# Performance work log

Hardware: AMD Instinct MI355X
Metric: run time of the kernel (lower is better)

## Reference

```python
import jax, jax.numpy as jnp
import numpy as np

EMBED_DIM = 1024
HEAD_DIM = 64


def setup_inputs() -> dict:
    key = jax.random.key(0)
    ks = jax.random.split(key, 7)
    B, S = 4, 2048
    x = jax.random.normal(ks[0], (B, S, EMBED_DIM), dtype=jnp.float32)
    s = EMBED_DIM ** -0.5  # torch Linear default init scale (uniform bound)
    Wk = jax.random.uniform(ks[1], (EMBED_DIM, HEAD_DIM), minval=-s, maxval=s)
    bk = jax.random.uniform(ks[2], (HEAD_DIM,), minval=-s, maxval=s)
    Wq = jax.random.uniform(ks[3], (EMBED_DIM, HEAD_DIM), minval=-s, maxval=s)
    bq = jax.random.uniform(ks[4], (HEAD_DIM,), minval=-s, maxval=s)
    Wv = jax.random.uniform(ks[5], (EMBED_DIM, HEAD_DIM), minval=-s, maxval=s)
    bv = jax.random.uniform(ks[6], (HEAD_DIM,), minval=-s, maxval=s)
    return {"x": x, "Wq": Wq, "bq": bq, "Wk": Wk, "bk": bk, "Wv": Wv, "bv": bv}


def reference(x, Wq, bq, Wk, bk, Wv, bv):
    # projections: [B,S,D]
    q = x @ Wq + bq
    k = x @ Wk + bk
    v = x @ Wv + bv
    # NOTE: faithful to source, which DIVIDES by head_dim**-0.5 (i.e. multiplies by sqrt(d))
    scale = HEAD_DIM ** -0.5
    wei = jnp.einsum('bqd,bkd->bqk', q, k) / scale  # [B,S,S]
    S = x.shape[1]
    causal = jnp.tril(jnp.ones((S, S), dtype=bool))
    wei = jnp.where(causal, wei, -jnp.inf)
    attn_weights = jax.nn.softmax(wei, axis=-1)
    return jnp.einsum('bqk,bkd->bqd', attn_weights, v)
```

## Files before the change

### kernel.cpp

```cpp
#include <hip/hip_runtime.h>
#include <math.h>

#define S_LEN 2048
#define NB 4
#define EMB 1024
#define HD 64
#define NROW (NB * S_LEN)
#define NEG_BIG -3.0e38f
#define SC 11.5415603f
#define DEFER_THR 3.0f
#define KVSPLIT 4

typedef _Float16 half8 __attribute__((ext_vector_type(8)));
typedef _Float16 half4 __attribute__((ext_vector_type(4)));
typedef float f32x4 __attribute__((ext_vector_type(4)));

static __device__ __forceinline__ f32x4 mfma32(half8 a, half8 b, f32x4 c) {
    return __builtin_amdgcn_mfma_f32_16x16x32_f16(a, b, c, 0, 0, 0);
}
static __device__ __forceinline__ f32x4 mfma16(half4 a, half4 b, f32x4 c) {
    return __builtin_amdgcn_mfma_f32_16x16x16f16(a, b, c, 0, 0, 0);
}

__global__ __launch_bounds__(256) void prep_w(
    const float* __restrict__ Wq, const float* __restrict__ Wk,
    const float* __restrict__ Wv, _Float16* __restrict__ wt_frag)
{
    const int g  = blockIdx.x >> 4;
    const int kc = blockIdx.x & 15;
    const int k0 = kc * 64;
    const float* W = (g == 0) ? Wq : (g == 1) ? Wk : Wv;

    __shared__ float tile[64][68];
    const int t = threadIdx.x;
    {
        const int kk = t >> 2, cb = (t & 3) * 16;
#pragma unroll
        for (int i = 0; i < 4; i++)
            *(f32x4*)&tile[kk][cb + 4 * i] =
                *(const f32x4*)(W + (size_t)(k0 + kk) * HD + cb + 4 * i);
    }
    __syncthreads();

    const int c4 = t >> 6, l = t & 63;
    const int col = c4 * 16 + (l & 15);
    const int krow = (l >> 4) * 8;
#pragma unroll
    for (int sub = 0; sub < 2; sub++) {
        half8 hv;
#pragma unroll
        for (int e = 0; e < 8; e++)
            hv[e] = (_Float16)tile[sub * 32 + krow + e][col];
        const size_t addr = (size_t)(g * 4 + c4) * 16384 +
                            (size_t)(kc * 2 + sub) * 512 + (size_t)l * 8;
        *(half8*)(wt_frag + addr) = hv;
    }
}

__global__ __launch_bounds__(768) void proj_kernel(
    const float* __restrict__ x, const _Float16* __restrict__ wt_frag,
    const float* __restrict__ bq, const float* __restrict__ bk,
    const float* __restrict__ bv,
    _Float16* __restrict__ qs, _Float16* __restrict__ kh_,
    _Float16* __restrict__ vt)
{
    const int m0 = blockIdx.x * 32;
    const int t = threadIdx.x, lane = t & 63, w = t >> 6;

    __shared__ __align__(16) _Float16 xs[32][1032];

    for (int i = t; i < 4096; i += 768) {
        const int row = i >> 7, off = (i & 127) * 8;
        const float* xp = x + (size_t)(m0 + row) * EMB + off;
        const f32x4 v0 = *(const f32x4*)xp;
        const f32x4 v1 = *(const f32x4*)(xp + 4);
        half8 h;
#pragma unroll
        for (int jj = 0; jj < 4; jj++) {
            h[jj]     = (_Float16)v0[jj];
            h[4 + jj] = (_Float16)v1[jj];
        }
        *(half8*)&xs[row][off] = h;
    }

    const int f = w;
    const int row0 = lane & 15, kq = lane >> 4;
    const _Float16* wp = wt_frag + (size_t)f * 16384 + (size_t)lane * 8;

    half8 wbuf[4];
#pragma unroll
    for (int c = 0; c < 4; c++) wbuf[c] = *(const half8*)(wp + (size_t)c * 512);

    __syncthreads();

    f32x4 acc0 = f32x4{0, 0, 0, 0}, acc1 = f32x4{0, 0, 0, 0};

#pragma unroll
    for (int c = 0; c < 32; ++c) {
        const half8 ax0 = *(const half8*)&xs[row0][c * 32 + kq * 8];
        const half8 ax1 = *(const half8*)&xs[16 + row0][c * 32 + kq * 8];
        const half8 bw = wbuf[c & 3];
        acc0 = mfma32(ax0, bw, acc0);
        acc1 = mfma32(ax1, bw, acc1);
        if (c + 4 < 32) wbuf[c & 3] = *(const half8*)(wp + (size_t)(c + 4) * 512);
    }

    const int mat = f >> 2, c4 = f & 3;
    const int mcol = c4 * 16 + (lane & 15);
    const float bb = ((mat == 0) ? bq : (mat == 1) ? bk : bv)[mcol];
#pragma unroll
    for (int rh = 0; rh < 2; rh++) {
        const f32x4 acc = rh ? acc1 : acc0;
        const int grow0 = m0 + rh * 16 + kq * 4;
        if (mat == 0) {
#pragma unroll
            for (int r = 0; r < 4; r++)
                qs[(size_t)(grow0 + r) * HD + mcol] = (_Float16)((acc[r] + bb) * SC);
        } else if (mat == 1) {
#pragma unroll
            for (int r = 0; r < 4; r++)
                kh_[(size_t)(grow0 + r) * HD + mcol] = (_Float16)(acc[r] + bb);
        } else {
            half4 hv;
#pragma unroll
            for (int r = 0; r < 4; r++) hv[r] = (_Float16)(acc[r] + bb);
            const int bidx = grow0 >> 11, sr = grow0 & (S_LEN - 1);
            *(half4*)(vt + ((size_t)bidx * HD + mcol) * S_LEN + sr) = hv;
        }
    }
}

__global__ __launch_bounds__(512) void attn_kernel(
    const _Float16* __restrict__ qs, const _Float16* __restrict__ kh_,
    const _Float16* __restrict__ vt,
    _Float16* __restrict__ po, float* __restrict__ pm, float* __restrict__ pl)
{
    const int id = blockIdx.x;
    const int qq = id & 3;
    const int b  = (id >> 2) & 3;
    const int qt = 31 - (id >> 4);
    const int q0 = qt * 64;
    const int t = threadIdx.x, lane = t & 63, w = t >> 6;
    const int rf = w >> 1, kvh = w & 1;

    __shared__ __align__(16) unsigned char smem[37888];
    _Float16 (*klds)[64][72] = (_Float16(*)[64][72])smem;
    _Float16 (*vlds)[64][72] = (_Float16(*)[64][72])(smem + 18432);
    float (*obuf)[16][68] = (float(*)[16][68])smem;
    float* mbuf = (float*)(smem + 36864);
    float* lbuf = (float*)(smem + 36864 + 512);

    const size_t rowq = ((size_t)b * S_LEN + q0 + rf * 16 + (lane & 15)) * HD + (lane >> 4) * 8;
    const half8 bq0 = *(const half8*)(qs + rowq);
    const half8 bq1 = *(const half8*)(qs + rowq + 32);

    f32x4 o[4];
#pragma unroll
    for (int c = 0; c < 4; c++) o[c] = f32x4{0, 0, 0, 0};
    float m_r = NEG_BIG, l_r = 0.f;

    const int nt = qt + 1;
    const int lo = (nt * qq) >> 2, hi = (nt * (qq + 1)) >> 2;

    const size_t kbase = (size_t)b * S_LEN * HD;
    const size_t vbase = (size_t)b * HD * S_LEN;
    const int srow = t >> 3, scol = (t & 7) * 8;

    half8 sK, sV;
    auto gload = [&](int tl) {
        sK = *(const half8*)(kh_ + kbase + (size_t)(tl * 64 + srow) * HD + scol);
        sV = *(const half8*)(vt + vbase + (size_t)srow * S_LEN + tl * 64 + scol);
    };
    auto swrite = [&](int nb) {
        *(half8*)&klds[nb][srow][scol] = sK;
        *(half8*)&vlds[nb][srow][scol] = sV;
    };

    if (lo < hi) { gload(lo); swrite(0); }
    __syncthreads();

    int cur = 0;
    for (int tl = lo; tl < hi; ++tl) {
        if (tl + 1 < hi) gload(tl + 1);

        const int kv0 = tl * 64 + kvh * 32;
        __builtin_amdgcn_s_setprio(1);
        f32x4 s[2];
#pragma unroll
        for (int h = 0; h < 2; h++) {
            const int keyl = kvh * 32 + 16 * h + (lane & 15);
            f32x4 a = f32x4{0, 0, 0, 0};
            a = mfma32(*(const half8*)&klds[cur][keyl][(lane >> 4) * 8], bq0, a);
            a = mfma32(*(const half8*)&klds[cur][keyl][32 + (lane >> 4) * 8], bq1, a);
            s[h] = a;
        }
        __builtin_amdgcn_s_setprio(0);

        const int qrow = q0 + rf * 16 + (lane & 15);
        const int kb0  = kv0 + (lane >> 4) * 4;
        float tv[8];
#pragma unroll
        for (int h = 0; h < 2; h++)
#pragma unroll
            for (int r = 0; r < 4; r++)
                tv[h * 4 + r] = (kb0 + 16 * h + r <= qrow) ? s[h][r] : NEG_BIG;

        float mt = tv[0];
#pragma unroll
        for (int i = 1; i < 8; i++) mt = fmaxf(mt, tv[i]);
        mt = fmaxf(mt, __shfl_xor(mt, 16));
        mt = fmaxf(mt, __shfl_xor(mt, 32));

        if (!__all(mt <= m_r + DEFER_THR)) {
            const float mn = fmaxf(m_r, mt);
            const float corr = exp2f(m_r - mn);
            m_r = mn;
            l_r *= corr;
            float corrB[4];
#pragma unroll
            for (int r = 0; r < 4; r++) corrB[r] = __shfl(corr, (lane >> 4) * 4 + r);
#pragma unroll
            for (int c = 0; c < 4; c++)
#pragma unroll
                for (int r = 0; r < 4; r++) o[c][r] *= corrB[r];
        }

        float p[8], rs = 0.f;
#pragma unroll
        for (int i = 0; i < 8; i++) { p[i] = exp2f(tv[i] - m_r); rs += p[i]; }
        rs += __shfl_xor(rs, 16);
        rs += __shfl_xor(rs, 32);
        l_r += rs;

        half4 pa[2];
#pragma unroll
        for (int h = 0; h < 2; h++)
#pragma unroll
            for (int r = 0; r < 4; r++) pa[h][r] = (_Float16)p[h * 4 + r];
        __builtin_amdgcn_s_setprio(1);
#pragma unroll
        for (int c = 0; c < 4; c++) {
#pragma unroll
            for (int h = 0; h < 2; h++) {
                const half4 vf = *(const half4*)&vlds[cur][16 * c + (lane & 15)]
                                                    [kvh * 32 + 16 * h + (lane >> 4) * 4];
                o[c] = mfma16(pa[h], vf, o[c]);
            }
        }
        __builtin_amdgcn_s_setprio(0);

        if (tl + 1 < hi) swrite(cur ^ 1);
        __syncthreads();
        cur ^= 1;
    }

    if (lane < 16) { mbuf[w * 16 + lane] = m_r; lbuf[w * 16 + lane] = l_r; }
#pragma unroll
    for (int c = 0; c < 4; c++)
#pragma unroll
        for (int r = 0; r < 4; r++)
            obuf[w][(lane >> 4) * 4 + r][16 * c + (lane & 15)] = o[c][r];
    __syncthreads();

    if (t < 256) {
        const int row16 = t >> 4, cb = (t & 15) * 4;
#pragma unroll
        for (int rf2 = 0; rf2 < 4; rf2++) {
            const int w0 = rf2 * 2, w1 = w0 + 1;
            const float m0v = mbuf[w0 * 16 + row16], m1v = mbuf[w1 * 16 + row16];
            const float M = fmaxf(m0v, m1v);
            const float e0 = exp2f(m0v - M), e1 = exp2f(m1v - M);
            const float L = lbuf[w0 * 16 + row16] * e0 + lbuf[w1 * 16 + row16] * e1;
            const f32x4 o0 = *(const f32x4*)&obuf[w0][row16][cb];
            const f32x4 o1 = *(const f32x4*)&obuf[w1][row16][cb];
            half4 hv;
#pragma unroll
            for (int jj = 0; jj < 4; jj++) hv[jj] = (_Float16)(o0[jj] * e0 + o1[jj] * e1);
            const size_t idx = (size_t)(qq * NB + b) * S_LEN + q0 + rf2 * 16 + row16;
            *(half4*)(po + idx * HD + cb) = hv;
            if ((t & 15) == 0) { pm[idx] = M; pl[idx] = L; }
        }
    }
}

__global__ __launch_bounds__(256) void merge_kernel(
    const _Float16* __restrict__ po, const float* __restrict__ pm,
    const float* __restrict__ pl, float* __restrict__ out)
{
    const int b = blockIdx.y;
    const int row = blockIdx.x * 16 + (threadIdx.x >> 4);
    const int cb = (threadIdx.x & 15) * 4;

    float mv[KVSPLIT];
    float M = NEG_BIG;
#pragma unroll
    for (int qq = 0; qq < KVSPLIT; qq++) {
        mv[qq] = pm[(size_t)(qq * NB + b) * S_LEN + row];
        M = fmaxf(M, mv[qq]);
    }
    float L = 0.f;
    f32x4 acc = f32x4{0, 0, 0, 0};
#pragma unroll
    for (int qq = 0; qq < KVSPLIT; qq++) {
        const size_t idx = (size_t)(qq * NB + b) * S_LEN + row;
        const float e = exp2f(mv[qq] - M);
        L += pl[idx] * e;
        const half4 ov = *(const half4*)(po + idx * HD + cb);
#pragma unroll
        for (int jj = 0; jj < 4; jj++) acc[jj] += (float)ov[jj] * e;
    }
    const float inv = 1.0f / L;
    f32x4 res;
#pragma unroll
    for (int jj = 0; jj < 4; jj++) res[jj] = acc[jj] * inv;
    *(f32x4*)(out + ((size_t)b * S_LEN + row) * HD + cb) = res;
}

extern "C" void kernel_launch(void* const* d_in, const int* in_sizes, int n_in,
                              void* d_out, int out_size, void* d_ws, size_t ws_size,
                              hipStream_t stream) {
    const float* x  = (const float*)d_in[0];
    const float* Wq = (const float*)d_in[1];
    const float* bq = (const float*)d_in[2];
    const float* Wk = (const float*)d_in[3];
    const float* bk = (const float*)d_in[4];
    const float* Wv = (const float*)d_in[5];
    const float* bv = (const float*)d_in[6];
    float* out = (float*)d_out;

    _Float16* ws = (_Float16*)d_ws;
    const size_t nW = (size_t)192 * EMB;
    const size_t n  = (size_t)NROW * HD;
    _Float16* wt_frag = ws;
    _Float16* qsb = wt_frag + nW;
    _Float16* khb = qsb + n;
    _Float16* vtb = khb + n;
    _Float16* po = vtb + n;
    float* pm = (float*)(po + (size_t)KVSPLIT * NB * S_LEN * HD);
    float* pl = pm + (size_t)KVSPLIT * NB * S_LEN;

    prep_w<<<48, 256, 0, stream>>>(Wq, Wk, Wv, wt_frag);
    proj_kernel<<<NROW / 32, 768, 0, stream>>>(
        x, wt_frag, bq, bk, bv, qsb, khb, vtb);
    attn_kernel<<<32 * NB * KVSPLIT, 512, 0, stream>>>(qsb, khb, vtb, po, pm, pl);
    merge_kernel<<<dim3(S_LEN / 16, NB), 256, 0, stream>>>(po, pm, pl, out);
}
```

Baseline: 36.73 us.

## Pipeline x loads in projection, double KV split, and halve prep_w tile size

The projection kernel stops staging the whole 32x1024 x tile before computing. It now double-buffers 256-column chunks, overlapping global loads and fp16 conversion with the MFMA loop. The attention KV split goes from 4 to 8, doubling the attention grid to add parallelism, at the cost of more partial outputs for the merge kernel to combine. prep_w is also split into twice as many smaller blocks.

```diff
diff --git a/kernel.cpp b/kernel.cpp
--- a/kernel.cpp
+++ b/kernel.cpp
@@ -9,7 +9,7 @@
 #define NEG_BIG -3.0e38f
 #define SC 11.5415603f
 #define DEFER_THR 3.0f
-#define KVSPLIT 4
+#define KVSPLIT 8
 
 typedef _Float16 half8 __attribute__((ext_vector_type(8)));
 typedef _Float16 half4 __attribute__((ext_vector_type(4)));
@@ -26,35 +26,28 @@
     const float* __restrict__ Wq, const float* __restrict__ Wk,
     const float* __restrict__ Wv, _Float16* __restrict__ wt_frag)
 {
-    const int g  = blockIdx.x >> 4;
-    const int kc = blockIdx.x & 15;
-    const int k0 = kc * 64;
+    const int g   = blockIdx.x >> 5;
+    const int c32 = blockIdx.x & 31;
+    const int k0  = c32 * 32;
     const float* W = (g == 0) ? Wq : (g == 1) ? Wk : Wv;
 
-    __shared__ float tile[64][68];
+    __shared__ float tile[32][68];
     const int t = threadIdx.x;
     {
-        const int kk = t >> 2, cb = (t & 3) * 16;
-#pragma unroll
-        for (int i = 0; i < 4; i++)
-            *(f32x4*)&tile[kk][cb + 4 * i] =
-                *(const f32x4*)(W + (size_t)(k0 + kk) * HD + cb + 4 * i);
+        const int kk = t >> 3, cb = (t & 7) * 8;
+        *(f32x4*)&tile[kk][cb]     = *(const f32x4*)(W + (size_t)(k0 + kk) * HD + cb);
+        *(f32x4*)&tile[kk][cb + 4] = *(const f32x4*)(W + (size_t)(k0 + kk) * HD + cb + 4);
     }
     __syncthreads();
 
     const int c4 = t >> 6, l = t & 63;
     const int col = c4 * 16 + (l & 15);
     const int krow = (l >> 4) * 8;
-#pragma unroll
-    for (int sub = 0; sub < 2; sub++) {
-        half8 hv;
-#pragma unroll
-        for (int e = 0; e < 8; e++)
-            hv[e] = (_Float16)tile[sub * 32 + krow + e][col];
-        const size_t addr = (size_t)(g * 4 + c4) * 16384 +
-                            (size_t)(kc * 2 + sub) * 512 + (size_t)l * 8;
-        *(half8*)(wt_frag + addr) = hv;
-    }
+    half8 hv;
+#pragma unroll
+    for (int e = 0; e < 8; e++) hv[e] = (_Float16)tile[krow + e][col];
+    *(half8*)(wt_frag + (size_t)(g * 4 + c4) * 16384 +
+              (size_t)c32 * 512 + (size_t)l * 8) = hv;
 }
 
 __global__ __launch_bounds__(768) void proj_kernel(
@@ -67,21 +60,7 @@
     const int m0 = blockIdx.x * 32;
     const int t = threadIdx.x, lane = t & 63, w = t >> 6;
 
-    __shared__ __align__(16) _Float16 xs[32][1032];
-
-    for (int i = t; i < 4096; i += 768) {
-        const int row = i >> 7, off = (i & 127) * 8;
-        const float* xp = x + (size_t)(m0 + row) * EMB + off;
-        const f32x4 v0 = *(const f32x4*)xp;
-        const f32x4 v1 = *(const f32x4*)(xp + 4);
-        half8 h;
-#pragma unroll
-        for (int jj = 0; jj < 4; jj++) {
-            h[jj]     = (_Float16)v0[jj];
-            h[4 + jj] = (_Float16)v1[jj];
-        }
-        *(half8*)&xs[row][off] = h;
-    }
+    __shared__ __align__(16) _Float16 xs[2][32][264];
 
     const int f = w;
     const int row0 = lane & 15, kq = lane >> 4;
@@ -91,18 +70,61 @@
 #pragma unroll
     for (int c = 0; c < 4; c++) wbuf[c] = *(const half8*)(wp + (size_t)c * 512);
 
+    const int g0r = t >> 5, g0c = (t & 31) * 8;
+    const int g1 = t + 768, g1r = g1 >> 5, g1c = (g1 & 31) * 8;
+
+    f32x4 sa0, sa1, sb0, sb1;
+    auto gloadX = [&](int ck) {
+        const float* p0 = x + (size_t)(m0 + g0r) * EMB + ck * 256 + g0c;
+        sa0 = *(const f32x4*)p0;
+        sa1 = *(const f32x4*)(p0 + 4);
+        if (t < 256) {
+            const float* p1 = x + (size_t)(m0 + g1r) * EMB + ck * 256 + g1c;
+            sb0 = *(const f32x4*)p1;
+            sb1 = *(const f32x4*)(p1 + 4);
+        }
+    };
+    auto swriteX = [&](int buf) {
+        half8 h;
+#pragma unroll
+        for (int jj = 0; jj < 4; jj++) {
+            h[jj]     = (_Float16)sa0[jj];
+            h[4 + jj] = (_Float16)sa1[jj];
+        }
+        *(half8*)&xs[buf][g0r][g0c] = h;
+        if (t < 256) {
+            half8 h2;
+#pragma unroll
+            for (int jj = 0; jj < 4; jj++) {
+                h2[jj]     = (_Float16)sb0[jj];
+                h2[4 + jj] = (_Float16)sb1[jj];
+            }
+            *(half8*)&xs[buf][g1r][g1c] = h2;
+        }
+    };
+
+    gloadX(0);
+    swriteX(0);
+    gloadX(1);
     __syncthreads();
 
     f32x4 acc0 = f32x4{0, 0, 0, 0}, acc1 = f32x4{0, 0, 0, 0};
 
-#pragma unroll
-    for (int c = 0; c < 32; ++c) {
-        const half8 ax0 = *(const half8*)&xs[row0][c * 32 + kq * 8];
-        const half8 ax1 = *(const half8*)&xs[16 + row0][c * 32 + kq * 8];
-        const half8 bw = wbuf[c & 3];
-        acc0 = mfma32(ax0, bw, acc0);
-        acc1 = mfma32(ax1, bw, acc1);
-        if (c + 4 < 32) wbuf[c & 3] = *(const half8*)(wp + (size_t)(c + 4) * 512);
+    for (int ck = 0; ck < 4; ++ck) {
+        const int buf = ck & 1;
+        if (ck + 1 < 4) swriteX(buf ^ 1);
+        if (ck + 2 < 4) gloadX(ck + 2);
+#pragma unroll
+        for (int s = 0; s < 8; ++s) {
+            const int c = ck * 8 + s;
+            const half8 ax0 = *(const half8*)&xs[buf][row0][s * 32 + kq * 8];
+            const half8 ax1 = *(const half8*)&xs[buf][16 + row0][s * 32 + kq * 8];
+            const half8 bw = wbuf[c & 3];
+            acc0 = mfma32(ax0, bw, acc0);
+            acc1 = mfma32(ax1, bw, acc1);
+            if (c + 4 < 32) wbuf[c & 3] = *(const half8*)(wp + (size_t)(c + 4) * 512);
+        }
+        __syncthreads();
     }
 
     const int mat = f >> 2, c4 = f & 3;
@@ -136,9 +158,9 @@
     _Float16* __restrict__ po, float* __restrict__ pm, float* __restrict__ pl)
 {
     const int id = blockIdx.x;
-    const int qq = id & 3;
-    const int b  = (id >> 2) & 3;
-    const int qt = 31 - (id >> 4);
+    const int qq = id & 7;
+    const int b  = (id >> 3) & 3;
+    const int qt = 31 - (id >> 5);
     const int q0 = qt * 64;
     const int t = threadIdx.x, lane = t & 63, w = t >> 6;
     const int rf = w >> 1, kvh = w & 1;
@@ -160,7 +182,7 @@
     float m_r = NEG_BIG, l_r = 0.f;
 
     const int nt = qt + 1;
-    const int lo = (nt * qq) >> 2, hi = (nt * (qq + 1)) >> 2;
+    const int lo = (nt * qq) >> 3, hi = (nt * (qq + 1)) >> 3;
 
     const size_t kbase = (size_t)b * S_LEN * HD;
     const size_t vbase = (size_t)b * HD * S_LEN;
@@ -339,7 +361,7 @@
     float* pm = (float*)(po + (size_t)KVSPLIT * NB * S_LEN * HD);
     float* pl = pm + (size_t)KVSPLIT * NB * S_LEN;
 
-    prep_w<<<48, 256, 0, stream>>>(Wq, Wk, Wv, wt_frag);
+    prep_w<<<96, 256, 0, stream>>>(Wq, Wk, Wv, wt_frag);
     proj_kernel<<<NROW / 32, 768, 0, stream>>>(
         x, wt_frag, bq, bk, bv, qsb, khb, vtb);
     attn_kernel<<<32 * NB * KVSPLIT, 512, 0, stream>>>(qsb, khb, vtb, po, pm, pl);
```

Result: slower. 40.14 us (+9.3%).
